# Optimization experiments

Hardware: AMD Instinct MI355X
Metric: run time of the kernel (lower is better)

## Reference

```python
import jax, jax.numpy as jnp
import numpy as np

B, L, H, Di, N, K, R = 2, 512, 2048, 4096, 16, 4, 128


def setup_inputs() -> dict:
    key = jax.random.key(0)
    ks = jax.random.split(key, 8)
    s = 0.02
    inp = {
        "x": jax.random.normal(ks[0], (B, L, H), jnp.float32),
        "in_w": jax.random.normal(ks[1], (2 * Di, H), jnp.float32) * s,
        "in_b": jnp.zeros((2 * Di,), jnp.float32),
        "conv_w": jax.random.normal(ks[2], (Di, 1, K), jnp.float32) * s,  # depthwise conv weight
        "conv_b": jnp.zeros((Di,), jnp.float32),
        "xproj_w": jax.random.normal(ks[3], (R + 2 * N, Di), jnp.float32) * s,
        "dt_w": jax.random.normal(ks[4], (Di, R), jnp.float32) * s,
        "dt_b": jax.random.normal(ks[5], (Di,), jnp.float32) * 0.1,
        "A_log": jnp.log(jnp.broadcast_to(jnp.arange(1, N + 1, dtype=jnp.float32)[None, :], (Di, N))) + jnp.zeros((Di, N), jnp.float32),
        "D": jnp.ones((Di,), jnp.float32),
        "out_w": jax.random.normal(ks[6], (H, Di), jnp.float32) * s,
        "out_b": jnp.zeros((H,), jnp.float32),
    }
    return inp


def reference(x, in_w, in_b, conv_w, conv_b, xproj_w, dt_w, dt_b, A_log, D, out_w, out_b):
    silu = jax.nn.silu
    # in_proj -> split into hidden path and gate
    proj = x @ in_w.T + in_b                       # [B, L, 2*Di]
    h, gate = jnp.split(proj, 2, axis=-1)          # each [B, L, Di]
    # causal depthwise conv1d over time
    hc = jnp.transpose(h, (0, 2, 1))               # [B, Di, L]
    hc = jax.lax.conv_general_dilated(
        hc, conv_w, window_strides=(1,), padding=[(K - 1, 0)],
        dimension_numbers=("NCH", "OIH", "NCH"), feature_group_count=Di)
    hc = silu(hc + conv_b[None, :, None])          # [B, Di, L]
    hs = jnp.transpose(hc, (0, 2, 1))              # [B, L, Di]
    # input-dependent SSM parameters
    sp = hs @ xproj_w.T                            # [B, L, R + 2N]
    ts, Bm, Cm = sp[..., :R], sp[..., R:R + N], sp[..., R + N:]
    dt = jax.nn.softplus(ts @ dt_w.T + dt_b)       # [B, L, Di]
    A = -jnp.exp(A_log)                            # [Di, N]
    dA = jnp.exp(dt[..., None] * A[None, None])    # [B, L, Di, N]
    dBu = dt[..., None] * Bm[:, :, None, :] * hs[..., None]  # [B, L, Di, N]

    # selective scan: s_t = dA_t * s_{t-1} + dBu_t ; y_t = s_t . C_t
    def step(s, inputs):
        dA_t, dBu_t, C_t = inputs                  # [B,Di,N], [B,Di,N], [B,N]
        s = dA_t * s + dBu_t
        y = jnp.einsum("bdn,bn->bd", s, C_t)
        return s, y

    s0 = jnp.zeros((x.shape[0], Di, N), x.dtype)
    _, ys = jax.lax.scan(step, s0, (jnp.swapaxes(dA, 0, 1), jnp.swapaxes(dBu, 0, 1), jnp.swapaxes(Cm, 0, 1)))
    y = jnp.transpose(ys, (1, 0, 2))               # [B, L, Di]
    y = (y + hs * D) * silu(gate)
    return y @ out_w.T + out_b                     # [B, L, H]
```

## Files before the change

kernel.cpp:

```cpp
#include <hip/hip_runtime.h>
#include <hip/hip_bf16.h>

typedef __hip_bfloat16 bf16;
typedef _Float16 fp16;
typedef short bf16x8 __attribute__((ext_vector_type(8)));
typedef float f32x4 __attribute__((ext_vector_type(4)));
typedef _Float16 half8 __attribute__((ext_vector_type(8)));
typedef _Float16 half2v __attribute__((ext_vector_type(2)));

#define BB 2
#define LL 512
#define HH 2048
#define DI 4096
#define NST 16
#define KK 4
#define RR 128
#define BLM (BB*LL)
#define CN 16
#define LC (LL/CN)
#define ZXP 16
#define ZOUT 4
#define CONV_N (BLM*DI)
#define CONV8_N (CONV_N/8)
#define CVT4_N (HH*DI/4)

enum { MODE_PROJ = 0, MODE_XPROJ = 1, MODE_DT = 2, MODE_OUT = 3 };

__device__ __forceinline__ float sigmoidf_(float x) { return 1.f / (1.f + __expf(-x)); }
__device__ __forceinline__ float softplusf_(float x) {
    return fmaxf(x, 0.f) + log1pf(__expf(-fabsf(x)));
}
__device__ __forceinline__ unsigned int bfpack(float a, float b) {
    __hip_bfloat162 h = __float22bfloat162_rn(make_float2(a, b));
    union { __hip_bfloat162 h; unsigned int u; } cv; cv.h = h;
    return cv.u;
}
__device__ __forceinline__ float b2f(short s) {
    union { unsigned u; float f; } c; c.u = ((unsigned)(unsigned short)s) << 16; return c.f;
}

typedef const __attribute__((address_space(1))) unsigned int* gas_t;
typedef __attribute__((address_space(3))) unsigned int* las_t;
__device__ __forceinline__ void gld16(const void* g, void* l) {
    __builtin_amdgcn_global_load_lds((gas_t)g, (las_t)l, 16, 0, 0);
}

__device__ __forceinline__ void cvt_seg(const float* s, bf16* d, int i) {
    float4 v = ((const float4*)s)[i];
    uint2 o; o.x = bfpack(v.x, v.y); o.y = bfpack(v.z, v.w);
    ((uint2*)d)[i] = o;
}

__global__ __launch_bounds__(256) void cvt_all(
    const float* __restrict__ s0, bf16* __restrict__ d0, int n0,
    const float* __restrict__ s1, bf16* __restrict__ d1, int n1,
    const float* __restrict__ s2, bf16* __restrict__ d2, int n2,
    const float* __restrict__ s3, bf16* __restrict__ d3, int n3)
{
    int i = blockIdx.x * 256 + threadIdx.x;
    int stride = gridDim.x * 256;
    int t1 = n0 + n1, t2 = t1 + n2, t3 = t2 + n3;
    for (; i < t3; i += stride) {
        if      (i < n0) cvt_seg(s0, d0, i);
        else if (i < t1) cvt_seg(s1, d1, i - n0);
        else if (i < t2) cvt_seg(s2, d2, i - t1);
        else             cvt_seg(s3, d3, i - t2);
    }
}

template<int BM, int BN, int MODE>
__global__ __launch_bounds__(256) void gemm_bf16(
    const bf16* __restrict__ A, const bf16* __restrict__ Bw,
    int N, int K, int lda, int ldb,
    const float* __restrict__ bias,
    bf16* __restrict__ outh, bf16* __restrict__ outh2,
    fp16* __restrict__ s0, fp16* __restrict__ s1,
    fp16* __restrict__ s2, fp16* __restrict__ s3)
{
    __shared__ short sA[BM * 64];
    __shared__ short sB[BN * 64];
    const int tid = threadIdx.x;
    const int col0 = blockIdx.x * BN;
    const int row0 = blockIdx.y * BM;
    const int wave = tid >> 6;
    const int lane = tid & 63;
    constexpr int NJR = (BM == 64 || BN == 64) ? 2 : 4;
    const int wr = (BM == 128) ? ((wave >> 1) * 64) : 0;
    const int wc = (BM == 64) ? (wave * 32) : ((wave & 1) * (BN / 2));
    const int lr = lane & 15;
    const int q  = lane >> 4;
    const int sw = lane & 7;

    const int kpb = K / gridDim.z;
    const int kbeg = blockIdx.z * kpb;
    const int kend = kbeg + kpb;

    const int r0 = tid >> 3;
    const int kc  = (tid & 7) << 3;
    const int kcs = (((tid & 7) ^ ((tid >> 3) & 7)) << 3);

    f32x4 acc[4][NJR] = {};

    for (int k0 = kbeg; k0 < kend; k0 += 64) {
        #pragma unroll
        for (int p = 0; p < BM / 32; p++) {
            int r = r0 + p * 32;
            gld16(A + (size_t)(row0 + r) * lda + k0 + kcs, &sA[r * 64 + kc]);
        }
        #pragma unroll
        for (int p = 0; p < BN / 32; p++) {
            int rr = r0 + p * 32;
            int nb = col0 + rr; if (nb > N - 1) nb = N - 1;
            gld16(Bw + (size_t)nb * ldb + k0 + kcs, &sB[rr * 64 + kc]);
        }
        __syncthreads();
        bf16x8 af[2][4], bfr[2][NJR];
        #pragma unroll
        for (int kk = 0; kk < 2; kk++) {
            const int cs = ((kk * 4 + q) ^ sw) << 3;
            #pragma unroll
            for (int i = 0; i < 4; i++)
                af[kk][i] = *(const bf16x8*)(&sA[(wr + i * 16 + lr) * 64 + cs]);
            #pragma unroll
            for (int j = 0; j < NJR; j++)
                bfr[kk][j] = *(const bf16x8*)(&sB[(wc + j * 16 + lr) * 64 + cs]);
        }
        #pragma unroll
        for (int kk = 0; kk < 2; kk++)
            #pragma unroll
            for (int i = 0; i < 4; i++)
                #pragma unroll
                for (int j = 0; j < NJR; j++)
                    acc[i][j] = __builtin_amdgcn_mfma_f32_16x16x32_bf16(af[kk][i], bfr[kk][j], acc[i][j], 0, 0, 0);
        __syncthreads();
    }

    fp16* oslice = s0;
    if (MODE == MODE_OUT) {
        int z = blockIdx.z;
        oslice = (z == 0) ? s0 : (z == 1) ? s1 : (z == 2) ? s2 : s3;
    }
    const int drow = (lane >> 4) << 2;
    const int dcol = lane & 15;
    #pragma unroll
    for (int i = 0; i < 4; i++) {
        #pragma unroll
        for (int j = 0; j < NJR; j++) {
            int n = col0 + wc + j * 16 + dcol;
            if (n >= N) continue;
            float bv = bias ? bias[n] : 0.f;
            #pragma unroll
            for (int r = 0; r < 4; r++) {
                int m = row0 + wr + i * 16 + drow + r;
                float v = acc[i][j][r];
                if (MODE == MODE_PROJ) {
                    v += bv;
                    if (n < DI) outh2[(size_t)m * DI + n] = (bf16)v;
                    else        outh[(size_t)m * DI + (n - DI)] = (bf16)v;
                } else if (MODE == MODE_XPROJ) {
                    s0[(size_t)blockIdx.z * (BLM * 160) + (size_t)m * 160 + n] = (fp16)v;
                } else if (MODE == MODE_DT) {
                    s0[(size_t)m * DI + n] = (fp16)softplusf_(v + bv);
                } else {
                    oslice[(size_t)m * HH + n] = (fp16)v;
                }
            }
        }
    }
}

__global__ __launch_bounds__(256) void conv_cvtow(
    const bf16* __restrict__ h, const float* __restrict__ conv_w,
    const float* __restrict__ conv_b, bf16* __restrict__ hs_b,
    const float* __restrict__ ow, bf16* __restrict__ ow_b)
{
    int i = blockIdx.x * 256 + threadIdx.x;
    int stride = gridDim.x * 256;
    for (; i < CONV8_N + CVT4_N; i += stride) {
        if (i < CONV8_N) {
            int idx = i << 3;
            int d0 = idx & (DI - 1);
            int l = (idx >> 12) & (LL - 1);
            float4 cb0 = *(const float4*)&conv_b[d0];
            float4 cb1 = *(const float4*)&conv_b[d0 + 4];
            float acc[8] = {cb0.x, cb0.y, cb0.z, cb0.w, cb1.x, cb1.y, cb1.z, cb1.w};
            float4 w[8];
            #pragma unroll
            for (int j = 0; j < 8; j++) w[j] = *(const float4*)&conv_w[(d0 + j) * KK];
            #pragma unroll
            for (int k = 0; k < KK; k++) {
                int ls = l - (KK - 1) + k;
                if (ls >= 0) {
                    bf16x8 hv = *(const bf16x8*)&h[(size_t)idx + (size_t)(ls - l) * DI];
                    #pragma unroll
                    for (int j = 0; j < 8; j++)
                        acc[j] += b2f(hv[j]) * ((const float*)&w[j])[k];
                }
            }
            uint4 o;
            float s0 = acc[0] * sigmoidf_(acc[0]), s1 = acc[1] * sigmoidf_(acc[1]);
            float s2 = acc[2] * sigmoidf_(acc[2]), s3 = acc[3] * sigmoidf_(acc[3]);
            float s4 = acc[4] * sigmoidf_(acc[4]), s5 = acc[5] * sigmoidf_(acc[5]);
            float s6 = acc[6] * sigmoidf_(acc[6]), s7 = acc[7] * sigmoidf_(acc[7]);
            o.x = bfpack(s0, s1); o.y = bfpack(s2, s3);
            o.z = bfpack(s4, s5); o.w = bfpack(s6, s7);
            *(uint4*)&hs_b[idx] = o;
        } else {
            cvt_seg(ow, ow_b, i - CONV8_N);
        }
    }
}

__global__ __launch_bounds__(256) void reduce_sp(
    const fp16* __restrict__ spS, float* __restrict__ sp_f, bf16* __restrict__ ts_b)
{
    int i = blockIdx.x * 256 + threadIdx.x;
    int row = i / 80, c2 = (i % 80) * 2;
    float r0 = 0.f, r1 = 0.f;
    #pragma unroll
    for (int z = 0; z < ZXP; z++) {
        half2v v = *(const half2v*)&spS[(size_t)z * (BLM * 160) + (size_t)row * 160 + c2];
        r0 += (float)v[0]; r1 += (float)v[1];
    }
    *(float2*)&sp_f[(size_t)row * 160 + c2] = make_float2(r0, r1);
    if (c2 < RR) *(unsigned*)&ts_b[(size_t)row * RR + c2] = bfpack(r0, r1);
}

__global__ __launch_bounds__(256) void reduce_out(
    const fp16* __restrict__ s0, const fp16* __restrict__ s1,
    const fp16* __restrict__ s2, const fp16* __restrict__ s3,
    const float* __restrict__ bias, float* __restrict__ out)
{
    int i = blockIdx.x * 256 + threadIdx.x;
    int c8 = (i & 255) << 3;
    half8 a = ((const half8*)s0)[i];
    half8 b = ((const half8*)s1)[i];
    half8 c = ((const half8*)s2)[i];
    half8 d = ((const half8*)s3)[i];
    float r[8];
    #pragma unroll
    for (int e = 0; e < 8; e++)
        r[e] = (float)a[e] + (float)b[e] + (float)c[e] + (float)d[e] + bias[c8 + e];
    ((float4*)out)[2 * i]     = make_float4(r[0], r[1], r[2], r[3]);
    ((float4*)out)[2 * i + 1] = make_float4(r[4], r[5], r[6], r[7]);
}

__global__ __launch_bounds__(256) void scan_part1(
    const fp16* __restrict__ dtr, const float* __restrict__ sp,
    const bf16* __restrict__ hs_b, const float* __restrict__ A_log,
    float* __restrict__ P_ws, float* __restrict__ S_ws)
{
    int bid = blockIdx.x;
    int c  = bid & (CN - 1);
    int db = (bid >> 4) & 63;
    int b  = bid >> 10;
    int ng = threadIdx.x >> 6;
    int d  = db * 64 + (threadIdx.x & 63);
    int n0 = ng * 4;

    float A[4], P[4], S[4];
    #pragma unroll
    for (int k = 0; k < 4; k++) {
        A[k] = -__expf(A_log[d * NST + n0 + k]);
        P[k] = 1.f; S[k] = 0.f;
    }
    const float* spb = sp + (size_t)b * LL * 160;
    size_t base = (size_t)b * LL * DI + d;
    for (int l = c * LC; l < (c + 1) * LC; l++) {
        size_t off = base + (size_t)l * DI;
        float dtv = (float)dtr[off];
        float hsv = (float)hs_b[off];
        float dh = dtv * hsv;
        #pragma unroll
        for (int k = 0; k < 4; k++) {
            float a  = __expf(dtv * A[k]);
            float Bn = spb[l * 160 + RR + n0 + k];
            S[k] = a * S[k] + dh * Bn;
            P[k] *= a;
        }
    }
    size_t ob = (size_t)(b * CN + c) * NST * DI + (size_t)n0 * DI + d;
    #pragma unroll
    for (int k = 0; k < 4; k++) {
        P_ws[ob + (size_t)k * DI] = P[k];
        S_ws[ob + (size_t)k * DI] = S[k];
    }
}

__global__ __launch_bounds__(256) void scan_mid(
    const float* __restrict__ P_ws, float* __restrict__ S_ws)
{
    int bid = blockIdx.x;
    int n  = bid & (NST - 1);
    int db = (bid >> 4) & (DI / 256 - 1);
    int b  = bid >> 8;
    int d  = db * 256 + threadIdx.x;
    size_t base = (size_t)n * DI + d;
    float s = 0.f;
    for (int c = 0; c < CN; c++) {
        size_t idx = (size_t)(b * CN + c) * NST * DI + base;
        float p  = P_ws[idx];
        float sv = S_ws[idx];
        S_ws[idx] = s;
        s = p * s + sv;
    }
}

__global__ __launch_bounds__(256) void scan_part2(
    const fp16* __restrict__ dtr, const float* __restrict__ sp,
    const bf16* __restrict__ hs_b, const bf16* __restrict__ g_b,
    const float* __restrict__ A_log, const float* __restrict__ Dv,
    const float* __restrict__ I_ws, bf16* __restrict__ y_b)
{
    __shared__ float yacc[4][LC][64];
    int bid = blockIdx.x;
    int c  = bid & (CN - 1);
    int db = (bid >> 4) & 63;
    int b  = bid >> 10;
    int w  = threadIdx.x >> 6;
    int lane = threadIdx.x & 63;
    int d  = db * 64 + lane;
    int n0 = w * 4;

    float A[4], s[4];
    #pragma unroll
    for (int k = 0; k < 4; k++)
        A[k] = -__expf(A_log[d * NST + n0 + k]);
    size_t ib = (size_t)(b * CN + c) * NST * DI + (size_t)n0 * DI + d;
    #pragma unroll
    for (int k = 0; k < 4; k++) s[k] = I_ws[ib + (size_t)k * DI];
    float Dd = Dv[d];

    const float* spb = sp + (size_t)b * LL * 160;
    size_t base = (size_t)b * LL * DI + d;
    for (int li = 0; li < LC; li++) {
        int l = c * LC + li;
        size_t off = base + (size_t)l * DI;
        float dtv = (float)dtr[off];
        float hsv = (float)hs_b[off];
        float dh = dtv * hsv;
        float y = 0.f;
        #pragma unroll
        for (int k = 0; k < 4; k++) {
            float a  = __expf(dtv * A[k]);
            float Bn = spb[l * 160 + RR + n0 + k];
            float Cn = spb[l * 160 + RR + NST + n0 + k];
            s[k] = a * s[k] + dh * Bn;
            y += s[k] * Cn;
        }
        if (w == 0) y += hsv * Dd;
        yacc[w][li][lane] = y;
    }
    __syncthreads();
    for (int t = threadIdx.x; t < LC * 64; t += 256) {
        int ll = t >> 6, dd = t & 63;
        float ysum = yacc[0][ll][dd] + yacc[1][ll][dd]
                   + yacc[2][ll][dd] + yacc[3][ll][dd];
        size_t off = (size_t)b * LL * DI + (size_t)(c * LC + ll) * DI + db * 64 + dd;
        float gv = (float)g_b[off];
        y_b[off] = (bf16)(ysum * (gv * sigmoidf_(gv)));
    }
}

extern "C" void kernel_launch(void* const* d_in, const int* in_sizes, int n_in,
                              void* d_out, int out_size, void* d_ws, size_t ws_size,
                              hipStream_t stream)
{
    const float* x       = (const float*)d_in[0];
    const float* in_w    = (const float*)d_in[1];
    const float* in_b    = (const float*)d_in[2];
    const float* conv_w  = (const float*)d_in[3];
    const float* conv_b  = (const float*)d_in[4];
    const float* xproj_w = (const float*)d_in[5];
    const float* dt_w    = (const float*)d_in[6];
    const float* dt_b    = (const float*)d_in[7];
    const float* A_log   = (const float*)d_in[8];
    const float* Dv      = (const float*)d_in[9];
    const float* out_w   = (const float*)d_in[10];
    const float* out_b   = (const float*)d_in[11];
    float* out = (float*)d_out;

    char* ws = (char*)d_ws;
    const size_t MB = 1u << 20;
    bf16*  h_b    = (bf16*)(ws);
    fp16*  spS    = (fp16*)(ws);
    float* P_ws   = (float*)(ws);
    fp16*  oS0    = (fp16*)(ws);
    fp16*  oS1    = (fp16*)(ws + 4 * MB);
    bf16*  x_b    = (bf16*)(ws + 8 * MB);
    float* S_ws   = (float*)(ws + 8 * MB);
    fp16*  oS2    = (fp16*)(ws + 8 * MB);
    fp16*  oS3    = (fp16*)(ws + 12 * MB);
    bf16*  in_w_b = (bf16*)(ws + 16 * MB);
    bf16*  ow_b   = (bf16*)(ws + 16 * MB);
    bf16*  y_b    = (bf16*)(ws + 32 * MB);
    fp16*  dt_h   = (fp16*)(ws + 40 * MB);
    bf16*  hs_b   = (bf16*)(ws + 48 * MB);
    bf16*  g_b    = (bf16*)(ws + 56 * MB);
    char* p = ws + 64 * MB;
    float* sp_f = (float*)p; p += (size_t)BLM * 160 * 4;
    bf16*  ts_b = (bf16*)p;  p += (size_t)BLM * RR * 2;
    bf16*  xw_b = (bf16*)p;  p += (size_t)(RR + 2 * NST) * DI * 2;
    bf16*  dtw_b= (bf16*)p;  p += (size_t)DI * RR * 2;

    cvt_all<<<2048, 256, 0, stream>>>(
        x, x_b, BLM * HH / 4,
        in_w, in_w_b, 2 * DI * HH / 4,
        xproj_w, xw_b, (RR + 2 * NST) * DI / 4,
        dt_w, dtw_b, DI * RR / 4);
    gemm_bf16<128, 64, MODE_PROJ><<<dim3((2 * DI) / 64, BLM / 128, 1), 256, 0, stream>>>(
        x_b, in_w_b, 2 * DI, HH, HH, HH, in_b, g_b, h_b,
        nullptr, nullptr, nullptr, nullptr);
    conv_cvtow<<<2048, 256, 0, stream>>>(h_b, conv_w, conv_b, hs_b, out_w, ow_b);
    gemm_bf16<64, 128, MODE_XPROJ><<<dim3(2, BLM / 64, ZXP), 256, 0, stream>>>(
        hs_b, xw_b, RR + 2 * NST, DI, DI, DI, nullptr, nullptr, nullptr,
        spS, nullptr, nullptr, nullptr);
    reduce_sp<<<320, 256, 0, stream>>>(spS, sp_f, ts_b);
    gemm_bf16<64, 128, MODE_DT><<<dim3(DI / 128, BLM / 64, 1), 256, 0, stream>>>(
        ts_b, dtw_b, DI, RR, RR, RR, dt_b, nullptr, nullptr,
        dt_h, nullptr, nullptr, nullptr);
    scan_part1<<<BB * (DI / 64) * CN, 256, 0, stream>>>(
        dt_h, sp_f, hs_b, A_log, P_ws, S_ws);
    scan_mid<<<BB * NST * (DI / 256), 256, 0, stream>>>(P_ws, S_ws);
    scan_part2<<<BB * (DI / 64) * CN, 256, 0, stream>>>(
        dt_h, sp_f, hs_b, g_b, A_log, Dv, S_ws, y_b);
    gemm_bf16<128, 128, MODE_OUT><<<dim3(HH / 128, BLM / 128, ZOUT), 256, 0, stream>>>(
        y_b, ow_b, HH, DI, DI, DI, nullptr, nullptr, nullptr,
        oS0, oS1, oS2, oS3);
    reduce_out<<<1024, 256, 0, stream>>>(oS0, oS1, oS2, oS3, out_b, out);
}
```

Before: 345.2 us.

## Double-buffer GEMM LDS tiles with async prefetch two steps ahead

The bf16 MFMA GEMM now keeps two LDS buffers for the A and B tiles and issues global_load_lds for tile t+2 while computing on tile t. Explicit s_waitcnt vmcnt and s_barrier replace the two __syncthreads per iteration, so global-load latency can overlap with MFMA work. This doubles LDS use per block, which may reduce occupancy. wait_vmcnt only emits a wait for counts 0, 6 and 8, so any tile shape with a different load count would skip the wait silently.

```diff
diff --git a/kernel.cpp b/kernel.cpp
--- a/kernel.cpp
+++ b/kernel.cpp
@@ -45,6 +45,14 @@
     __builtin_amdgcn_global_load_lds((gas_t)g, (las_t)l, 16, 0, 0);
 }
 
+template<int N_>
+__device__ __forceinline__ void wait_vmcnt() {
+    if constexpr (N_ == 0)      asm volatile("s_waitcnt vmcnt(0)" ::: "memory");
+    else if constexpr (N_ == 6) asm volatile("s_waitcnt vmcnt(6)" ::: "memory");
+    else if constexpr (N_ == 8) asm volatile("s_waitcnt vmcnt(8)" ::: "memory");
+    __builtin_amdgcn_sched_barrier(0);
+}
+
 __device__ __forceinline__ void cvt_seg(const float* s, bf16* d, int i) {
     float4 v = ((const float4*)s)[i];
     uint2 o; o.x = bfpack(v.x, v.y); o.y = bfpack(v.z, v.w);
@@ -77,14 +85,15 @@
     fp16* __restrict__ s0, fp16* __restrict__ s1,
     fp16* __restrict__ s2, fp16* __restrict__ s3)
 {
-    __shared__ short sA[BM * 64];
-    __shared__ short sB[BN * 64];
+    __shared__ short sA[2][BM * 64];
+    __shared__ short sB[2][BN * 64];
     const int tid = threadIdx.x;
     const int col0 = blockIdx.x * BN;
     const int row0 = blockIdx.y * BM;
     const int wave = tid >> 6;
     const int lane = tid & 63;
     constexpr int NJR = (BM == 64 || BN == 64) ? 2 : 4;
+    constexpr int LPS = BM / 32 + BN / 32;
     const int wr = (BM == 128) ? ((wave >> 1) * 64) : 0;
     const int wc = (BM == 64) ? (wave * 32) : ((wave & 1) * (BN / 2));
     const int lr = lane & 15;
@@ -93,37 +102,47 @@
 
     const int kpb = K / gridDim.z;
     const int kbeg = blockIdx.z * kpb;
-    const int kend = kbeg + kpb;
+    const int NT = kpb >> 6;
 
     const int r0 = tid >> 3;
     const int kc  = (tid & 7) << 3;
     const int kcs = (((tid & 7) ^ ((tid >> 3) & 7)) << 3);
 
-    f32x4 acc[4][NJR] = {};
-
-    for (int k0 = kbeg; k0 < kend; k0 += 64) {
+    auto stage = [&](int buf, int k0) {
         #pragma unroll
         for (int p = 0; p < BM / 32; p++) {
             int r = r0 + p * 32;
-            gld16(A + (size_t)(row0 + r) * lda + k0 + kcs, &sA[r * 64 + kc]);
+            gld16(A + (size_t)(row0 + r) * lda + k0 + kcs, &sA[buf][r * 64 + kc]);
         }
         #pragma unroll
         for (int p = 0; p < BN / 32; p++) {
             int rr = r0 + p * 32;
             int nb = col0 + rr; if (nb > N - 1) nb = N - 1;
-            gld16(Bw + (size_t)nb * ldb + k0 + kcs, &sB[rr * 64 + kc]);
-        }
-        __syncthreads();
+            gld16(Bw + (size_t)nb * ldb + k0 + kcs, &sB[buf][rr * 64 + kc]);
+        }
+    };
+
+    f32x4 acc[4][NJR] = {};
+
+    stage(0, kbeg);
+    stage(1, kbeg + 64);
+    wait_vmcnt<LPS>();
+    __builtin_amdgcn_s_barrier();
+
+    for (int t = 0; t < NT; t++) {
+        const int cur = t & 1;
+        const short* pA = sA[cur];
+        const short* pB = sB[cur];
         bf16x8 af[2][4], bfr[2][NJR];
         #pragma unroll
         for (int kk = 0; kk < 2; kk++) {
             const int cs = ((kk * 4 + q) ^ sw) << 3;
             #pragma unroll
             for (int i = 0; i < 4; i++)
-                af[kk][i] = *(const bf16x8*)(&sA[(wr + i * 16 + lr) * 64 + cs]);
+                af[kk][i] = *(const bf16x8*)(&pA[(wr + i * 16 + lr) * 64 + cs]);
             #pragma unroll
             for (int j = 0; j < NJR; j++)
-                bfr[kk][j] = *(const bf16x8*)(&sB[(wc + j * 16 + lr) * 64 + cs]);
+                bfr[kk][j] = *(const bf16x8*)(&pB[(wc + j * 16 + lr) * 64 + cs]);
         }
         #pragma unroll
         for (int kk = 0; kk < 2; kk++)
@@ -132,7 +151,16 @@
                 #pragma unroll
                 for (int j = 0; j < NJR; j++)
                     acc[i][j] = __builtin_amdgcn_mfma_f32_16x16x32_bf16(af[kk][i], bfr[kk][j], acc[i][j], 0, 0, 0);
-        __syncthreads();
+
+        __builtin_amdgcn_s_barrier();
+        if (t + 2 < NT) {
+            stage(cur, kbeg + (t + 2) * 64);
+            wait_vmcnt<LPS>();
+        } else {
+            wait_vmcnt<0>();
+        }
+        __builtin_amdgcn_s_barrier();
+        __builtin_amdgcn_sched_barrier(0);
     }
 
     fp16* oslice = s0;
```

Measured after the change: 353.8 us. +2.5%, slower.
